# Optimization experiments

Hardware: AMD Instinct MI355X
Metric: run time of the kernel (lower is better)

## Reference

```python
import jax, jax.numpy as jnp
import numpy as np

N_QUBITS = 4
DIM = 2 ** N_QUBITS  # 16
N_LAYERS = 3

# PennyLane default.qubit convention: wire 0 is the most-significant bit.

def _cnot_perm(c, t):
    # CNOT is a basis permutation (involution): flip target bit where control bit is 1
    idx = np.arange(DIM)
    cbit = (idx >> (N_QUBITS - 1 - c)) & 1
    return np.where(cbit == 1, idx ^ (1 << (N_QUBITS - 1 - t)), idx)

# BasicEntanglerLayers ring: CNOT(0,1), CNOT(1,2), CNOT(2,3), CNOT(3,0)
CNOT_PERMS = [jnp.asarray(_cnot_perm(q, (q + 1) % N_QUBITS)) for q in range(N_QUBITS)]
# PauliZ sign table: Z_SIGNS[i, q] = +1 if bit q of basis state i is 0 else -1
Z_SIGNS = jnp.asarray(np.array([[1.0 - 2.0 * ((i >> (N_QUBITS - 1 - q)) & 1)
                                 for q in range(N_QUBITS)] for i in range(DIM)], dtype=np.float32))


def _ry(theta):
    # RY(t) = [[cos t/2, -sin t/2], [sin t/2, cos t/2]] ; theta [...] -> [..., 2, 2] complex64
    c, s = jnp.cos(theta / 2), jnp.sin(theta / 2)
    m = jnp.stack([jnp.stack([c, -s], -1), jnp.stack([s, c], -1)], -2)
    return m.astype(jnp.complex64)


def _rx(theta):
    # RX(t) = [[cos t/2, -i sin t/2], [-i sin t/2, cos t/2]]
    c, s = jnp.cos(theta / 2), jnp.sin(theta / 2)
    z = jnp.zeros_like(c)
    real = jnp.stack([jnp.stack([c, z], -1), jnp.stack([z, c], -1)], -2)
    imag = jnp.stack([jnp.stack([z, -s], -1), jnp.stack([-s, z], -1)], -2)
    return (real + 1j * imag).astype(jnp.complex64)


def _apply_1q(state, gate, q, batched):
    # state [B, 16]; gate [B,2,2] (batched) or [2,2]; apply on qubit q
    B = state.shape[0]
    a, b = 2 ** q, 2 ** (N_QUBITS - 1 - q)
    s = state.reshape(B, a, 2, b)
    if batched:
        s = jnp.einsum('bij,bajc->baic', gate, s)
    else:
        s = jnp.einsum('ij,bajc->baic', gate, s)
    return s.reshape(B, DIM)


def _circuit(inputs, weights):
    B = inputs.shape[0]
    state = jnp.zeros((B, DIM), jnp.complex64).at[:, 0].set(1.0)  # |0000>
    ry = _ry(inputs)  # [B, 4, 2, 2] AngleEmbedding (rotation='Y')
    for q in range(N_QUBITS):
        state = _apply_1q(state, ry[:, q], q, batched=True)
    rx = _rx(weights)  # [3, 4, 2, 2] BasicEntanglerLayers (RX per qubit)
    for l in range(N_LAYERS):
        for q in range(N_QUBITS):
            state = _apply_1q(state, rx[l, q], q, batched=False)
        for q in range(N_QUBITS):  # ring of CNOTs
            state = state[:, CNOT_PERMS[q]]
    probs = state.real ** 2 + state.imag ** 2  # [B, 16]
    return probs @ Z_SIGNS  # [B, 4] PauliZ expectations


def setup_inputs() -> dict:
    key = jax.random.key(0)
    k1, k2 = jax.random.split(key)
    B = 1048576
    inputs = jax.random.normal(k1, (B, N_QUBITS), dtype=jnp.float32)
    weights = jax.random.normal(k2, (N_LAYERS, N_QUBITS), dtype=jnp.float32) * 0.05  # random_normal init
    return {"inputs": inputs, "weights": weights}


def reference(inputs, weights):
    return _circuit(inputs, weights)
```

## Files before the change

### kernel.cpp

```cpp
#include <hip/hip_runtime.h>

#define NQ 4
#define DIM 16
#define NL 3

__global__ void qlayer_prep(const float* __restrict__ w, float* __restrict__ ws) {
    int i = threadIdx.x;
    if (i < NL * NQ) {
        float t = 0.5f * w[i];
        ws[i]           = cosf(t);
        ws[i + NL * NQ] = sinf(t);
    }
}

__global__ __launch_bounds__(256) void qlayer_main(const float* __restrict__ inputs,
                                                   const float* __restrict__ wcs,
                                                   float* __restrict__ out, int B) {
    int b = blockIdx.x * blockDim.x + threadIdx.x;
    if (b >= B) return;

    float cw[NL * NQ], sw[NL * NQ];
#pragma unroll
    for (int i = 0; i < NL * NQ; ++i) {
        cw[i] = wcs[i];
        sw[i] = wcs[i + NL * NQ];
    }

    float4 in = reinterpret_cast<const float4*>(inputs)[b];
    float ci[NQ], si[NQ];
    {
        float a;
        a = 0.5f * in.x; ci[0] = __cosf(a); si[0] = __sinf(a);
        a = 0.5f * in.y; ci[1] = __cosf(a); si[1] = __sinf(a);
        a = 0.5f * in.z; ci[2] = __cosf(a); si[2] = __sinf(a);
        a = 0.5f * in.w; ci[3] = __cosf(a); si[3] = __sinf(a);
    }

    float re[DIM], im[DIM];
#pragma unroll
    for (int i = 0; i < DIM; ++i) {
        float v = ((i >> 3) & 1) ? si[0] : ci[0];
        v      *= ((i >> 2) & 1) ? si[1] : ci[1];
        v      *= ((i >> 1) & 1) ? si[2] : ci[2];
        v      *= ((i >> 0) & 1) ? si[3] : ci[3];
        re[i] = v;
        im[i] = 0.0f;
    }

#pragma unroll
    for (int l = 0; l < NL; ++l) {
#pragma unroll
        for (int q = 0; q < NQ; ++q) {
            float c = cw[l * NQ + q];
            float s = sw[l * NQ + q];
            const int tbit = 1 << (3 - q);
#pragma unroll
            for (int i = 0; i < DIM; ++i) {
                if (!(i & tbit)) {
                    const int j = i | tbit;
                    float r0 = re[i], i0 = im[i];
                    float r1 = re[j], i1 = im[j];
                    re[i] = c * r0 + s * i1;
                    im[i] = c * i0 - s * r1;
                    re[j] = c * r1 + s * i0;
                    im[j] = c * i1 - s * r0;
                }
            }
        }
#pragma unroll
        for (int q = 0; q < NQ; ++q) {
            const int cbit = 1 << (3 - q);
            const int tbit = 1 << (3 - ((q + 1) % NQ));
            float nr[DIM], ni[DIM];
#pragma unroll
            for (int i = 0; i < DIM; ++i) {
                const int j = (i & cbit) ? (i ^ tbit) : i;
                nr[i] = re[j];
                ni[i] = im[j];
            }
#pragma unroll
            for (int i = 0; i < DIM; ++i) {
                re[i] = nr[i];
                im[i] = ni[i];
            }
        }
    }

    float p[DIM];
#pragma unroll
    for (int i = 0; i < DIM; ++i) p[i] = re[i] * re[i] + im[i] * im[i];

    float oq[NQ];
#pragma unroll
    for (int q = 0; q < NQ; ++q) {
        float acc = 0.0f;
#pragma unroll
        for (int i = 0; i < DIM; ++i) {
            acc = ((i >> (3 - q)) & 1) ? (acc - p[i]) : (acc + p[i]);
        }
        oq[q] = acc;
    }
    reinterpret_cast<float4*>(out)[b] = make_float4(oq[0], oq[1], oq[2], oq[3]);
}

extern "C" void kernel_launch(void* const* d_in, const int* in_sizes, int n_in,
                              void* d_out, int out_size, void* d_ws, size_t ws_size,
                              hipStream_t stream) {
    const float* inputs  = (const float*)d_in[0];
    const float* weights = (const float*)d_in[1];
    float* out = (float*)d_out;
    float* wcs = (float*)d_ws;

    const int B = in_sizes[0] / NQ;

    qlayer_prep<<<1, 64, 0, stream>>>(weights, wcs);
    qlayer_main<<<(B + 255) / 256, 256, 0, stream>>>(inputs, wcs, out, B);
}
```

Before: 89.44 us.

## Fuse weight prep into main kernel and process four samples per thread

Removes the separate prep kernel launch by computing the weight cos/sin in every thread with fast intrinsics. Each thread now handles four batch elements, which amortizes that trig cost and cuts the grid size. It also factors the initial product state through pairwise products and computes the Z expectations with a butterfly reduction to save arithmetic. The risks are lower precision from __cosf/__sinf on the weights and fewer waves in flight per element.

```diff
diff --git a/kernel.cpp b/kernel.cpp
--- a/kernel.cpp
+++ b/kernel.cpp
@@ -3,104 +3,110 @@
 #define NQ 4
 #define DIM 16
 #define NL 3
+#define EPT 4
+#define BLK 256
 
-__global__ void qlayer_prep(const float* __restrict__ w, float* __restrict__ ws) {
-    int i = threadIdx.x;
-    if (i < NL * NQ) {
-        float t = 0.5f * w[i];
-        ws[i]           = cosf(t);
-        ws[i + NL * NQ] = sinf(t);
-    }
-}
-
-__global__ __launch_bounds__(256) void qlayer_main(const float* __restrict__ inputs,
-                                                   const float* __restrict__ wcs,
-                                                   float* __restrict__ out, int B) {
-    int b = blockIdx.x * blockDim.x + threadIdx.x;
-    if (b >= B) return;
-
+__global__ __launch_bounds__(BLK) void qlayer_fused(const float* __restrict__ inputs,
+                                                    const float* __restrict__ weights,
+                                                    float* __restrict__ out, int B) {
     float cw[NL * NQ], sw[NL * NQ];
 #pragma unroll
     for (int i = 0; i < NL * NQ; ++i) {
-        cw[i] = wcs[i];
-        sw[i] = wcs[i + NL * NQ];
+        float t = 0.5f * weights[i];
+        cw[i] = __cosf(t);
+        sw[i] = __sinf(t);
     }
 
-    float4 in = reinterpret_cast<const float4*>(inputs)[b];
-    float ci[NQ], si[NQ];
-    {
-        float a;
-        a = 0.5f * in.x; ci[0] = __cosf(a); si[0] = __sinf(a);
-        a = 0.5f * in.y; ci[1] = __cosf(a); si[1] = __sinf(a);
-        a = 0.5f * in.z; ci[2] = __cosf(a); si[2] = __sinf(a);
-        a = 0.5f * in.w; ci[3] = __cosf(a); si[3] = __sinf(a);
-    }
-
-    float re[DIM], im[DIM];
-#pragma unroll
-    for (int i = 0; i < DIM; ++i) {
-        float v = ((i >> 3) & 1) ? si[0] : ci[0];
-        v      *= ((i >> 2) & 1) ? si[1] : ci[1];
-        v      *= ((i >> 1) & 1) ? si[2] : ci[2];
-        v      *= ((i >> 0) & 1) ? si[3] : ci[3];
-        re[i] = v;
-        im[i] = 0.0f;
-    }
+    const int base = blockIdx.x * (BLK * EPT) + threadIdx.x;
 
 #pragma unroll
-    for (int l = 0; l < NL; ++l) {
+    for (int e = 0; e < EPT; ++e) {
+        const int b = base + e * BLK;
+        if (b >= B) continue;
+
+        float4 in = reinterpret_cast<const float4*>(inputs)[b];
+        float ci[NQ], si[NQ];
+        {
+            float a;
+            a = 0.5f * in.x; ci[0] = __cosf(a); si[0] = __sinf(a);
+            a = 0.5f * in.y; ci[1] = __cosf(a); si[1] = __sinf(a);
+            a = 0.5f * in.z; ci[2] = __cosf(a); si[2] = __sinf(a);
+            a = 0.5f * in.w; ci[3] = __cosf(a); si[3] = __sinf(a);
+        }
+
+        float f01[4], f23[4];
+        f01[0] = ci[0] * ci[1]; f01[1] = ci[0] * si[1];
+        f01[2] = si[0] * ci[1]; f01[3] = si[0] * si[1];
+        f23[0] = ci[2] * ci[3]; f23[1] = ci[2] * si[3];
+        f23[2] = si[2] * ci[3]; f23[3] = si[2] * si[3];
+
+        float re[DIM], im[DIM];
 #pragma unroll
-        for (int q = 0; q < NQ; ++q) {
-            float c = cw[l * NQ + q];
-            float s = sw[l * NQ + q];
-            const int tbit = 1 << (3 - q);
+        for (int i = 0; i < DIM; ++i) {
+            re[i] = f01[i >> 2] * f23[i & 3];
+            im[i] = 0.0f;
+        }
+
 #pragma unroll
-            for (int i = 0; i < DIM; ++i) {
-                if (!(i & tbit)) {
-                    const int j = i | tbit;
-                    float r0 = re[i], i0 = im[i];
-                    float r1 = re[j], i1 = im[j];
-                    re[i] = c * r0 + s * i1;
-                    im[i] = c * i0 - s * r1;
-                    re[j] = c * r1 + s * i0;
-                    im[j] = c * i1 - s * r0;
+        for (int l = 0; l < NL; ++l) {
+#pragma unroll
+            for (int q = 0; q < NQ; ++q) {
+                const float c = cw[l * NQ + q];
+                const float s = sw[l * NQ + q];
+                const int tbit = 1 << (3 - q);
+#pragma unroll
+                for (int i = 0; i < DIM; ++i) {
+                    if (!(i & tbit)) {
+                        const int j = i | tbit;
+                        float r0 = re[i], i0 = im[i];
+                        float r1 = re[j], i1 = im[j];
+                        re[i] = c * r0 + s * i1;
+                        im[i] = c * i0 - s * r1;
+                        re[j] = c * r1 + s * i0;
+                        im[j] = c * i1 - s * r0;
+                    }
+                }
+            }
+#pragma unroll
+            for (int q = 0; q < NQ; ++q) {
+                const int cbit = 1 << (3 - q);
+                const int tbit = 1 << (3 - ((q + 1) % NQ));
+                float nr[DIM], ni[DIM];
+#pragma unroll
+                for (int i = 0; i < DIM; ++i) {
+                    const int j = (i & cbit) ? (i ^ tbit) : i;
+                    nr[i] = re[j];
+                    ni[i] = im[j];
+                }
+#pragma unroll
+                for (int i = 0; i < DIM; ++i) {
+                    re[i] = nr[i];
+                    im[i] = ni[i];
                 }
             }
         }
+
+        float p[DIM];
 #pragma unroll
-        for (int q = 0; q < NQ; ++q) {
-            const int cbit = 1 << (3 - q);
-            const int tbit = 1 << (3 - ((q + 1) % NQ));
-            float nr[DIM], ni[DIM];
+        for (int i = 0; i < DIM; ++i) p[i] = re[i] * re[i] + im[i] * im[i];
+
+        float s1[8], z3 = 0.0f;
 #pragma unroll
-            for (int i = 0; i < DIM; ++i) {
-                const int j = (i & cbit) ? (i ^ tbit) : i;
-                nr[i] = re[j];
-                ni[i] = im[j];
-            }
+        for (int k = 0; k < 8; ++k) {
+            s1[k] = p[2 * k] + p[2 * k + 1];
+            z3 += p[2 * k] - p[2 * k + 1];
+        }
+        float s2[4], z2 = 0.0f;
 #pragma unroll
-            for (int i = 0; i < DIM; ++i) {
-                re[i] = nr[i];
-                im[i] = ni[i];
-            }
+        for (int k = 0; k < 4; ++k) {
+            s2[k] = s1[2 * k] + s1[2 * k + 1];
+            z2 += s1[2 * k] - s1[2 * k + 1];
         }
+        float z1 = (s2[0] - s2[1]) + (s2[2] - s2[3]);
+        float z0 = (s2[0] + s2[1]) - (s2[2] + s2[3]);
+
+        reinterpret_cast<float4*>(out)[b] = make_float4(z0, z1, z2, z3);
     }
-
-    float p[DIM];
-#pragma unroll
-    for (int i = 0; i < DIM; ++i) p[i] = re[i] * re[i] + im[i] * im[i];
-
-    float oq[NQ];
-#pragma unroll
-    for (int q = 0; q < NQ; ++q) {
-        float acc = 0.0f;
-#pragma unroll
-        for (int i = 0; i < DIM; ++i) {
-            acc = ((i >> (3 - q)) & 1) ? (acc - p[i]) : (acc + p[i]);
-        }
-        oq[q] = acc;
-    }
-    reinterpret_cast<float4*>(out)[b] = make_float4(oq[0], oq[1], oq[2], oq[3]);
 }
 
 extern "C" void kernel_launch(void* const* d_in, const int* in_sizes, int n_in,
@@ -109,10 +115,9 @@
     const float* inputs  = (const float*)d_in[0];
     const float* weights = (const float*)d_in[1];
     float* out = (float*)d_out;
-    float* wcs = (float*)d_ws;
 
     const int B = in_sizes[0] / NQ;
+    const int grid = (B + BLK * EPT - 1) / (BLK * EPT);
 
-    qlayer_prep<<<1, 64, 0, stream>>>(weights, wcs);
-    qlayer_main<<<(B + 255) / 256, 256, 0, stream>>>(inputs, wcs, out, B);
+    qlayer_fused<<<grid, BLK, 0, stream>>>(inputs, weights, out, B);
 }
```

Result: faster. 81.75 us (-8.6%).
